# Kernel optimization log

Hardware: AMD Instinct MI355X
Metric: run time of the kernel (lower is better)

## Reference

```python
import jax, jax.numpy as jnp
import numpy as np

N_NODES = 50000


def _add_self_loops(edge_index, n):
    loop = jnp.arange(n, dtype=edge_index.dtype)
    src = jnp.concatenate([edge_index[0], loop])
    dst = jnp.concatenate([edge_index[1], loop])
    return src, dst


def _gcn_norm(src, dst, n):
    # symmetric normalization with unit edge weights (edge_weight=None)
    w = jnp.ones(src.shape[0], dtype=jnp.float32)
    deg = jax.ops.segment_sum(w, dst, num_segments=n)  # [N]
    dinv = jnp.where(deg > 0, jax.lax.rsqrt(jnp.maximum(deg, 1.0)), 0.0)
    return dinv[src] * w * dinv[dst]  # [E+N]


def _gcn_conv(x, src, dst, norm, W, b, n):
    h = x @ W                                   # [N, out] transform first (PyG order)
    msg = h[src] * norm[:, None]                # [E+N, out] gather + scale
    agg = jax.ops.segment_sum(msg, dst, num_segments=n)  # scatter-add
    return agg + b


def setup_inputs() -> dict:
    key = jax.random.key(0)
    k1, k2, k3, k4 = jax.random.split(key, 4)
    N, E, IN, HID, OUT = N_NODES, 1600000, 512, 64, 7
    x = jax.random.normal(k1, (N, IN), dtype=jnp.float32)
    edge_index = jax.random.randint(k2, (2, E), 0, N, dtype=jnp.int64)
    W1 = jax.random.normal(k3, (IN, HID), dtype=jnp.float32) * (1.0 / np.sqrt(IN))
    b1 = jnp.zeros((HID,), dtype=jnp.float32)
    W2 = jax.random.normal(k4, (HID, OUT), dtype=jnp.float32) * (1.0 / np.sqrt(HID))
    b2 = jnp.zeros((OUT,), dtype=jnp.float32)
    return {"x": x, "edge_index": edge_index, "W1": W1, "b1": b1, "W2": W2, "b2": b2}


def reference(x, edge_index, W1, b1, W2, b2):
    n = x.shape[0]
    src, dst = _add_self_loops(edge_index, n)
    norm = _gcn_norm(src, dst, n)  # graph-only, shared across layers
    h = _gcn_conv(x, src, dst, norm, W1, b1, n)
    h = jax.nn.relu(h)
    # dropout is identity in eval/inference mode
    out = _gcn_conv(h, src, dst, norm, W2, b2, n)
    return out
```

## Files before the change

kernel.cpp:

```cpp
#include <hip/hip_runtime.h>

#define N_NODES 50000
#define N_EDGES 1600000
#define DIM_IN  512
#define DIM_HID 64
#define DIM_OUT 7
#define NBUCK   196
#define PART_BLOCKS 256
#define BCAP    16384

using u16 = unsigned short;
using bf16x8 = __attribute__((ext_vector_type(8))) __bf16;
using f32x4  = __attribute__((ext_vector_type(4))) float;

__device__ __forceinline__ float bf2f(u16 u) {
    union { float f; unsigned int i; } v;
    v.i = ((unsigned int)u) << 16;
    return v.f;
}

__device__ __forceinline__ u16 f2bf(float f) {
    union { float f; unsigned int i; } v;
    v.f = f;
    unsigned int r = 0x7FFFu + ((v.i >> 16) & 1u);
    return (u16)((v.i + r) >> 16);
}

__device__ __forceinline__ float bflo(unsigned int u) {
    union { float f; unsigned int i; } v;
    v.i = u << 16;
    return v.f;
}

__device__ __forceinline__ float bfhi(unsigned int u) {
    union { float f; unsigned int i; } v;
    v.i = u & 0xFFFF0000u;
    return v.f;
}

__device__ __forceinline__ int ld_edge(const int* ei, int i64f, size_t idx) {
    if (i64f) return ei[2 * idx];
    return ei[idx];
}

__global__ void k_detect(const u16* __restrict__ xw, const int* __restrict__ ei32,
                         int* __restrict__ flags, int* __restrict__ gcnt) {
    __shared__ int s1[256];
    __shared__ int s2[256];
    int t = threadIdx.x;
    u16 w = xw[2 * t];
    int e = (w >> 7) & 0xFF;
    s1[t] = (e >= 100 && e <= 140) ? 1 : 0;
    s2[t] = (ei32[2 * t + 1] != 0) ? 1 : 0;
    if (t < NBUCK) gcnt[t] = 0;
    __syncthreads();
    for (int off = 128; off >= 1; off >>= 1) {
        if (t < off) { s1[t] += s1[t + off]; s2[t] += s2[t + off]; }
        __syncthreads();
    }
    if (t == 0) {
        flags[0] = (s1[0] >= 200) ? 0 : 1;
        flags[1] = (s2[0] == 0) ? 1 : 0;
    }
}

__launch_bounds__(1024)
__global__ void k_scat(const int* __restrict__ ei, const int* __restrict__ flags,
                       int* __restrict__ gcnt, unsigned int* __restrict__ ebuf) {
    __shared__ int hist[NBUCK];
    __shared__ int cur[NBUCK];
    int t = threadIdx.x, blk = blockIdx.x;
    int i64f = flags[1];
    const int CH = (N_EDGES + PART_BLOCKS - 1) / PART_BLOCKS;
    int lo = blk * CH;
    int hi = lo + CH; if (hi > N_EDGES) hi = N_EDGES;
    if (t < NBUCK) hist[t] = 0;
    __syncthreads();
    for (int i = lo + t; i < hi; i += 1024) {
        int s = ld_edge(ei, i64f, (size_t)i);
        int d = ld_edge(ei, i64f, (size_t)N_EDGES + i);
        if ((unsigned)d < (unsigned)N_NODES && (unsigned)s < (unsigned)N_NODES)
            atomicAdd(&hist[d >> 8], 1);
    }
    __syncthreads();
    if (t < NBUCK) {
        int h = hist[t];
        cur[t] = (h > 0) ? atomicAdd(&gcnt[t], h) : 0;
    }
    __syncthreads();
    for (int i = lo + t; i < hi; i += 1024) {
        int s = ld_edge(ei, i64f, (size_t)i);
        int d = ld_edge(ei, i64f, (size_t)N_EDGES + i);
        if ((unsigned)d < (unsigned)N_NODES && (unsigned)s < (unsigned)N_NODES) {
            int b = d >> 8;
            int off = atomicAdd(&cur[b], 1);
            if ((unsigned)off < (unsigned)BCAP)
                ebuf[(size_t)b * BCAP + off] = ((unsigned)s << 8) | (unsigned)(d & 255);
        }
    }
}

__launch_bounds__(1024)
__global__ void k_cfill(const unsigned int* __restrict__ ebuf,
                        const int* __restrict__ gcnt,
                        int* __restrict__ rowptr, float* __restrict__ dinv,
                        int* __restrict__ col) {
    __shared__ int gs[256];
    __shared__ int dcnt[256];
    __shared__ int sc[256];
    __shared__ int cur[256];
    int b = blockIdx.x, t = threadIdx.x;
    if (t < 256) {
        int gv = (t < NBUCK) ? gcnt[t] : 0;
        if (gv > BCAP) gv = BCAP;
        gs[t] = gv;
    }
    __syncthreads();
    for (int off = 1; off < 256; off <<= 1) {
        int u = (t >= off && t < 256) ? gs[t - off] : 0;
        __syncthreads();
        if (t < 256) gs[t] += u;
        __syncthreads();
    }
    int cntb = gcnt[b]; if (cntb > BCAP) cntb = BCAP;
    int cb = gs[b] - cntb;
    if (b == 0 && t == 0) rowptr[N_NODES] = gs[255];
    const unsigned int* eb = ebuf + (size_t)b * BCAP;

    if (t < 256) dcnt[t] = 0;
    __syncthreads();
    for (int e = t; e < cntb; e += 1024)
        atomicAdd(&dcnt[eb[e] & 255u], 1);
    __syncthreads();
    int v = 0;
    if (t < 256) { v = dcnt[t]; sc[t] = v; }
    __syncthreads();
    for (int off = 1; off < 256; off <<= 1) {
        int u = (t >= off && t < 256) ? sc[t - off] : 0;
        __syncthreads();
        if (t < 256) sc[t] += u;
        __syncthreads();
    }
    if (t < 256) {
        int row0 = cb + sc[t] - v;
        cur[t] = row0;
        int idx = b * 256 + t;
        if (idx < N_NODES) {
            rowptr[idx] = row0;
            dinv[idx] = rsqrtf((float)(v + 1));
        }
    }
    __syncthreads();
    for (int e = t; e < cntb; e += 1024) {
        unsigned int x = eb[e];
        int p = atomicAdd(&cur[x & 255u], 1);
        if ((unsigned)p < (unsigned)N_EDGES) col[p] = (int)(x >> 8);
    }
}

__global__ void k_tw1(const void* __restrict__ W1, const int* __restrict__ flags,
                      u16* __restrict__ W1T) {
    int i = blockIdx.x * blockDim.x + threadIdx.x;
    if (i < DIM_IN * DIM_HID) {
        int n = i >> 9;
        int k = i & 511;
        if (flags[0]) W1T[i] = f2bf(((const float*)W1)[k * DIM_HID + n]);
        else          W1T[i] = ((const u16*)W1)[k * DIM_HID + n];
    }
}

__launch_bounds__(256)
__global__ void k_gemm1(const void* __restrict__ xraw, const u16* __restrict__ W1T,
                        const int* __restrict__ flags, const float* __restrict__ dinv,
                        u16* __restrict__ hs) {
    int f32f = flags[0];
    int wave = threadIdx.x >> 6;
    int lane = threadIdx.x & 63;
    int m16 = lane & 15;
    int quad = lane >> 4;
    int rbase = blockIdx.x * 64 + wave * 16;
    int ra = rbase + m16;
    if (ra > N_NODES - 1) ra = N_NODES - 1;
    const u16*   xrow_b = (const u16*)xraw   + (size_t)ra * DIM_IN + quad * 8;
    const float* xrow_f = (const float*)xraw + (size_t)ra * DIM_IN + quad * 8;
    const u16* wrow = W1T + (size_t)m16 * DIM_IN + quad * 8;

    f32x4 acc0 = {0.f, 0.f, 0.f, 0.f};
    f32x4 acc1 = {0.f, 0.f, 0.f, 0.f};
    f32x4 acc2 = {0.f, 0.f, 0.f, 0.f};
    f32x4 acc3 = {0.f, 0.f, 0.f, 0.f};

    for (int ks = 0; ks < DIM_IN / 32; ++ks) {
        bf16x8 a;
        if (f32f) {
            const float4* q = reinterpret_cast<const float4*>(xrow_f + ks * 32);
            float4 p0 = q[0], p1 = q[1];
            union { bf16x8 v; u16 s[8]; } u;
            u.s[0] = f2bf(p0.x); u.s[1] = f2bf(p0.y); u.s[2] = f2bf(p0.z); u.s[3] = f2bf(p0.w);
            u.s[4] = f2bf(p1.x); u.s[5] = f2bf(p1.y); u.s[6] = f2bf(p1.z); u.s[7] = f2bf(p1.w);
            a = u.v;
        } else {
            a = *reinterpret_cast<const bf16x8*>(xrow_b + ks * 32);
        }
        bf16x8 b0 = *reinterpret_cast<const bf16x8*>(wrow + ks * 32);
        bf16x8 b1 = *reinterpret_cast<const bf16x8*>(wrow + ks * 32 + 16 * DIM_IN);
        bf16x8 b2 = *reinterpret_cast<const bf16x8*>(wrow + ks * 32 + 32 * DIM_IN);
        bf16x8 b3 = *reinterpret_cast<const bf16x8*>(wrow + ks * 32 + 48 * DIM_IN);
        acc0 = __builtin_amdgcn_mfma_f32_16x16x32_bf16(a, b0, acc0, 0, 0, 0);
        acc1 = __builtin_amdgcn_mfma_f32_16x16x32_bf16(a, b1, acc1, 0, 0, 0);
        acc2 = __builtin_amdgcn_mfma_f32_16x16x32_bf16(a, b2, acc2, 0, 0, 0);
        acc3 = __builtin_amdgcn_mfma_f32_16x16x32_bf16(a, b3, acc3, 0, 0, 0);
    }

#pragma unroll
    for (int i = 0; i < 4; ++i) {
        int r = rbase + quad * 4 + i;
        if (r < N_NODES) {
            float dv = dinv[r];
            u16* orow = hs + (size_t)r * DIM_HID;
            orow[ 0 + m16] = f2bf(acc0[i] * dv);
            orow[16 + m16] = f2bf(acc1[i] * dv);
            orow[32 + m16] = f2bf(acc2[i] * dv);
            orow[48 + m16] = f2bf(acc3[i] * dv);
        }
    }
}

__launch_bounds__(256)
__global__ void k_agg1(const u16* __restrict__ hs, const int* __restrict__ rowptr,
                       const int* __restrict__ col, const float* __restrict__ dinv,
                       const void* __restrict__ b1, const void* __restrict__ W2,
                       const int* __restrict__ flags, float* __restrict__ zs) {
    __shared__ float xh[4][64];
    int f32f = flags[0];
    int wave = threadIdx.x >> 6;
    int lane = threadIdx.x & 63;
    int g = lane >> 3;
    int q = lane & 7;
    int d = blockIdx.x * 4 + wave;
    int start = rowptr[d], end = rowptr[d + 1];
    if (start < 0) start = 0;
    if (end > N_EDGES) end = N_EDGES;
    if (end < start) end = start;

    float a[8];
#pragma unroll
    for (int k = 0; k < 8; ++k) a[k] = 0.f;

    const uint4* hs4 = reinterpret_cast<const uint4*>(hs);
    const int* cp = col + start;
    int ne = end - start;
    int nfull = ne >> 3;

    int it = 0;
    for (; it + 4 <= nfull; it += 4) {
        int c0 = cp[(it + 0) * 8 + g];
        int c1 = cp[(it + 1) * 8 + g];
        int c2 = cp[(it + 2) * 8 + g];
        int c3 = cp[(it + 3) * 8 + g];
        uint4 r0 = hs4[(size_t)c0 * 8 + q];
        uint4 r1 = hs4[(size_t)c1 * 8 + q];
        uint4 r2 = hs4[(size_t)c2 * 8 + q];
        uint4 r3 = hs4[(size_t)c3 * 8 + q];
#pragma unroll
        for (int u = 0; u < 4; ++u) {
            uint4 r = (u == 0) ? r0 : (u == 1) ? r1 : (u == 2) ? r2 : r3;
            a[0] += bflo(r.x); a[1] += bfhi(r.x);
            a[2] += bflo(r.y); a[3] += bfhi(r.y);
            a[4] += bflo(r.z); a[5] += bfhi(r.z);
            a[6] += bflo(r.w); a[7] += bfhi(r.w);
        }
    }
    for (; it < nfull; ++it) {
        int c = cp[it * 8 + g];
        uint4 r = hs4[(size_t)c * 8 + q];
        a[0] += bflo(r.x); a[1] += bfhi(r.x);
        a[2] += bflo(r.y); a[3] += bfhi(r.y);
        a[4] += bflo(r.z); a[5] += bfhi(r.z);
        a[6] += bflo(r.w); a[7] += bfhi(r.w);
    }
    {
        int e = start + nfull * 8 + g;
        if (e < end) {
            int c = col[e];
            uint4 r = hs4[(size_t)c * 8 + q];
            a[0] += bflo(r.x); a[1] += bfhi(r.x);
            a[2] += bflo(r.y); a[3] += bfhi(r.y);
            a[4] += bflo(r.z); a[5] += bfhi(r.z);
            a[6] += bflo(r.w); a[7] += bfhi(r.w);
        }
    }

#pragma unroll
    for (int k = 0; k < 8; ++k) {
        a[k] += __shfl_xor(a[k], 8);
        a[k] += __shfl_xor(a[k], 16);
        a[k] += __shfl_xor(a[k], 32);
    }

    {
        uint4 r = hs4[(size_t)d * 8 + q];
        a[0] += bflo(r.x); a[1] += bfhi(r.x);
        a[2] += bflo(r.y); a[3] += bfhi(r.y);
        a[4] += bflo(r.z); a[5] += bfhi(r.z);
        a[6] += bflo(r.w); a[7] += bfhi(r.w);
    }

    float dv = dinv[d];
    float h[8];
    if (f32f) {
        const float* bf = (const float*)b1 + q * 8;
#pragma unroll
        for (int k = 0; k < 8; ++k) h[k] = fmaxf(a[k] * dv + bf[k], 0.f);
    } else {
        const u16* bb = (const u16*)b1 + q * 8;
#pragma unroll
        for (int k = 0; k < 8; ++k) h[k] = fmaxf(a[k] * dv + bf2f(bb[k]), 0.f);
    }

    if (g == 0) {
#pragma unroll
        for (int k = 0; k < 8; ++k) xh[wave][q * 8 + k] = h[k];
    }
    __syncthreads();
    float h2 = xh[wave][lane];

    float p[7];
#pragma unroll
    for (int f = 0; f < 7; ++f) {
        float w = f32f ? ((const float*)W2)[lane * DIM_OUT + f]
                       : bf2f(((const u16*)W2)[lane * DIM_OUT + f]);
        p[f] = h2 * w;
    }
#pragma unroll
    for (int off = 32; off >= 1; off >>= 1) {
#pragma unroll
        for (int f = 0; f < 7; ++f) p[f] += __shfl_xor(p[f], off);
    }
    if (lane == 0) {
#pragma unroll
        for (int f = 0; f < 7; ++f) zs[(size_t)d * 8 + f] = p[f] * dv;
        zs[(size_t)d * 8 + 7] = 0.f;
    }
}

__launch_bounds__(256)
__global__ void k_agg2(const float* __restrict__ zs, const int* __restrict__ rowptr,
                       const int* __restrict__ col, const float* __restrict__ dinv,
                       const void* __restrict__ b2, const int* __restrict__ flags,
                       float* __restrict__ out) {
    int f32f = flags[0];
    int wave = threadIdx.x >> 6;
    int lane = threadIdx.x & 63;
    int d = blockIdx.x * 4 + wave;
    if (d >= N_NODES) return;
    int f = lane & 7;
    int g = lane >> 3;
    int start = rowptr[d], end = rowptr[d + 1];
    if (start < 0) start = 0;
    if (end > N_EDGES) end = N_EDGES;
    if (end < start) end = start;

    float acc = 0.f;
    for (int e = start + g; e < end; e += 8)
        acc += zs[(size_t)col[e] * 8 + f];

    acc += __shfl_xor(acc, 8);
    acc += __shfl_xor(acc, 16);
    acc += __shfl_xor(acc, 32);

    if (lane < 7) {
        float b2v = f32f ? ((const float*)b2)[lane] : bf2f(((const u16*)b2)[lane]);
        float tot = (acc + zs[(size_t)d * 8 + lane]) * dinv[d] + b2v;
        out[(size_t)d * DIM_OUT + lane] = tot;
    }
}

extern "C" void kernel_launch(void* const* d_in, const int* in_sizes, int n_in,
                              void* d_out, int out_size, void* d_ws, size_t ws_size,
                              hipStream_t stream) {
    const void* x  = d_in[0];
    const int*  ei = (const int*)d_in[1];
    const void* W1 = d_in[2];
    const void* b1 = d_in[3];
    const void* W2 = d_in[4];
    const void* b2 = d_in[5];

    char* ws = (char*)d_ws;
    size_t off = 0;
    auto alloc = [&](size_t bytes) -> void* {
        void* p = ws + off;
        off = (off + bytes + 255) & ~(size_t)255;
        return p;
    };
    int*   flags  = (int*)alloc(32);
    int*   rowptr = (int*)alloc((size_t)(N_NODES + 1) * 4);
    int*   gcnt   = (int*)alloc((size_t)NBUCK * 4);
    float* dinv   = (float*)alloc((size_t)N_NODES * 4);
    u16*   W1T    = (u16*)alloc((size_t)DIM_IN * DIM_HID * 2);
    unsigned int* ebuf = (unsigned int*)alloc((size_t)NBUCK * BCAP * 4);
    int*   colb   = (int*)alloc((size_t)N_EDGES * 4);
    u16*   hs     = (u16*)alloc((size_t)N_NODES * DIM_HID * 2);
    float* zs     = (float*)alloc((size_t)N_NODES * 8 * 4);
    float* out    = (float*)d_out;

    k_detect<<<1, 256, 0, stream>>>((const u16*)x, ei, flags, gcnt);
    k_scat  <<<PART_BLOCKS, 1024, 0, stream>>>(ei, flags, gcnt, ebuf);
    k_cfill <<<NBUCK, 1024, 0, stream>>>(ebuf, gcnt, rowptr, dinv, colb);
    k_tw1   <<<(DIM_IN * DIM_HID + 255) / 256, 256, 0, stream>>>(W1, flags, W1T);
    k_gemm1 <<<(N_NODES + 63) / 64, 256, 0, stream>>>(x, W1T, flags, dinv, hs);
    k_agg1  <<<(N_NODES + 3) / 4, 256, 0, stream>>>(hs, rowptr, colb, dinv, b1, W2, flags, zs);
    k_agg2  <<<(N_NODES + 3) / 4, 256, 0, stream>>>(zs, rowptr, colb, dinv, b2, flags, out);
}
```

Measured before the change: 290.2 us.

## Fuse detect into W1 transpose, drop LDS reduction in agg1, batch col loads in agg2

Merges the dtype-detection kernel into the W1 transpose kernel, so each of 32 blocks recomputes the flag and one launch disappears. agg1 computes the second-layer projection per lane-group with a short 8-lane shuffle reduction, removing the shared-memory staging, the __syncthreads, and the full 64-lane reduction. agg2 loads 64 column indices at once per wave, broadcasts them with shuffles, and issues 8 independent gathers per thread to expose more memory-level parallelism. The trade-offs are redundant detection work in every block and more W2 loads per lane in agg1.

```diff
diff --git a/kernel.cpp b/kernel.cpp
--- a/kernel.cpp
+++ b/kernel.cpp
@@ -43,24 +43,41 @@
     return ei[idx];
 }
 
-__global__ void k_detect(const u16* __restrict__ xw, const int* __restrict__ ei32,
-                         int* __restrict__ flags, int* __restrict__ gcnt) {
+__launch_bounds__(1024)
+__global__ void k_tw1(const u16* __restrict__ xw, const int* __restrict__ ei32,
+                      const void* __restrict__ W1, int* __restrict__ flags,
+                      int* __restrict__ gcnt, u16* __restrict__ W1T) {
     __shared__ int s1[256];
     __shared__ int s2[256];
+    __shared__ int f32s;
     int t = threadIdx.x;
-    u16 w = xw[2 * t];
-    int e = (w >> 7) & 0xFF;
-    s1[t] = (e >= 100 && e <= 140) ? 1 : 0;
-    s2[t] = (ei32[2 * t + 1] != 0) ? 1 : 0;
-    if (t < NBUCK) gcnt[t] = 0;
+    if (t < 256) {
+        u16 w = xw[2 * t];
+        int e = (w >> 7) & 0xFF;
+        s1[t] = (e >= 100 && e <= 140) ? 1 : 0;
+        s2[t] = (ei32[2 * t + 1] != 0) ? 1 : 0;
+    }
     __syncthreads();
     for (int off = 128; off >= 1; off >>= 1) {
         if (t < off) { s1[t] += s1[t + off]; s2[t] += s2[t + off]; }
         __syncthreads();
     }
-    if (t == 0) {
-        flags[0] = (s1[0] >= 200) ? 0 : 1;
-        flags[1] = (s2[0] == 0) ? 1 : 0;
+    if (t == 0) f32s = (s1[0] >= 200) ? 0 : 1;
+    if (blockIdx.x == 0) {
+        if (t == 0) {
+            flags[0] = (s1[0] >= 200) ? 0 : 1;
+            flags[1] = (s2[0] == 0) ? 1 : 0;
+        }
+        if (t < NBUCK) gcnt[t] = 0;
+    }
+    __syncthreads();
+    int f32f = f32s;
+    int i = blockIdx.x * 1024 + t;
+    if (i < DIM_IN * DIM_HID) {
+        int n = i >> 9;
+        int k = i & 511;
+        if (f32f) W1T[i] = f2bf(((const float*)W1)[k * DIM_HID + n]);
+        else      W1T[i] = ((const u16*)W1)[k * DIM_HID + n];
     }
 }
 
@@ -155,17 +172,6 @@
         unsigned int x = eb[e];
         int p = atomicAdd(&cur[x & 255u], 1);
         if ((unsigned)p < (unsigned)N_EDGES) col[p] = (int)(x >> 8);
-    }
-}
-
-__global__ void k_tw1(const void* __restrict__ W1, const int* __restrict__ flags,
-                      u16* __restrict__ W1T) {
-    int i = blockIdx.x * blockDim.x + threadIdx.x;
-    if (i < DIM_IN * DIM_HID) {
-        int n = i >> 9;
-        int k = i & 511;
-        if (flags[0]) W1T[i] = f2bf(((const float*)W1)[k * DIM_HID + n]);
-        else          W1T[i] = ((const u16*)W1)[k * DIM_HID + n];
     }
 }
 
@@ -231,7 +237,6 @@
                        const int* __restrict__ col, const float* __restrict__ dinv,
                        const void* __restrict__ b1, const void* __restrict__ W2,
                        const int* __restrict__ flags, float* __restrict__ zs) {
-    __shared__ float xh[4][64];
     int f32f = flags[0];
     int wave = threadIdx.x >> 6;
     int lane = threadIdx.x & 63;
@@ -318,24 +323,27 @@
         for (int k = 0; k < 8; ++k) h[k] = fmaxf(a[k] * dv + bf2f(bb[k]), 0.f);
     }
 
-    if (g == 0) {
-#pragma unroll
-        for (int k = 0; k < 8; ++k) xh[wave][q * 8 + k] = h[k];
-    }
-    __syncthreads();
-    float h2 = xh[wave][lane];
-
     float p[7];
 #pragma unroll
+    for (int f = 0; f < 7; ++f) p[f] = 0.f;
+    if (f32f) {
+        const float* w2 = (const float*)W2 + q * 8 * DIM_OUT;
+#pragma unroll
+        for (int k = 0; k < 8; ++k)
+#pragma unroll
+            for (int f = 0; f < 7; ++f) p[f] += h[k] * w2[k * DIM_OUT + f];
+    } else {
+        const u16* w2 = (const u16*)W2 + q * 8 * DIM_OUT;
+#pragma unroll
+        for (int k = 0; k < 8; ++k)
+#pragma unroll
+            for (int f = 0; f < 7; ++f) p[f] += h[k] * bf2f(w2[k * DIM_OUT + f]);
+    }
+#pragma unroll
     for (int f = 0; f < 7; ++f) {
-        float w = f32f ? ((const float*)W2)[lane * DIM_OUT + f]
-                       : bf2f(((const u16*)W2)[lane * DIM_OUT + f]);
-        p[f] = h2 * w;
-    }
-#pragma unroll
-    for (int off = 32; off >= 1; off >>= 1) {
-#pragma unroll
-        for (int f = 0; f < 7; ++f) p[f] += __shfl_xor(p[f], off);
+        p[f] += __shfl_xor(p[f], 1);
+        p[f] += __shfl_xor(p[f], 2);
+        p[f] += __shfl_xor(p[f], 4);
     }
     if (lane == 0) {
 #pragma unroll
@@ -362,8 +370,19 @@
     if (end < start) end = start;
 
     float acc = 0.f;
-    for (int e = start + g; e < end; e += 8)
-        acc += zs[(size_t)col[e] * 8 + f];
+    for (int base = start; base < end; base += 64) {
+        int rem = end - base; if (rem > 64) rem = 64;
+        int ce = base + lane;
+        int c = (ce < end) ? col[ce] : 0;
+        float vv[8];
+#pragma unroll
+        for (int j = 0; j < 8; ++j) {
+            int cj = __shfl(c, j * 8 + g);
+            vv[j] = (j * 8 + g < rem) ? zs[(size_t)cj * 8 + f] : 0.f;
+        }
+#pragma unroll
+        for (int j = 0; j < 8; ++j) acc += vv[j];
+    }
 
     acc += __shfl_xor(acc, 8);
     acc += __shfl_xor(acc, 16);
@@ -404,10 +423,9 @@
     float* zs     = (float*)alloc((size_t)N_NODES * 8 * 4);
     float* out    = (float*)d_out;
 
-    k_detect<<<1, 256, 0, stream>>>((const u16*)x, ei, flags, gcnt);
+    k_tw1   <<<32, 1024, 0, stream>>>((const u16*)x, ei, W1, flags, gcnt, W1T);
     k_scat  <<<PART_BLOCKS, 1024, 0, stream>>>(ei, flags, gcnt, ebuf);
     k_cfill <<<NBUCK, 1024, 0, stream>>>(ebuf, gcnt, rowptr, dinv, colb);
-    k_tw1   <<<(DIM_IN * DIM_HID + 255) / 256, 256, 0, stream>>>(W1, flags, W1T);
     k_gemm1 <<<(N_NODES + 63) / 64, 256, 0, stream>>>(x, W1T, flags, dinv, hs);
     k_agg1  <<<(N_NODES + 3) / 4, 256, 0, stream>>>(hs, rowptr, colb, dinv, b1, W2, flags, zs);
     k_agg2  <<<(N_NODES + 3) / 4, 256, 0, stream>>>(zs, rowptr, colb, dinv, b2, flags, out);
```

After: 294.8 us. No clear change (+1.6%).
